# Kernel optimization log

Measured on AMD Instinct MI355X. Metric: run time of the kernel, lower is better.

The kernel has to match this reference:

```python
import jax, jax.numpy as jnp
import numpy as np

B, T, D, H = 16, 256, 128, 256  # batch, max_len, input_size, hidden_size (= attention hidden)


def _gru(x_seq, h0, Wih, Whh, bih, bhh):
    """Torch-style GRU over time. x_seq: [B,T,H_in], h0: [B,H]. Returns outputs [B,T,H], hT [B,H]."""
    x_proj = jnp.einsum('bti,gi->btg', x_seq, Wih) + bih  # [B,T,3H], precompute input projections

    def step(h, xp):
        gi_r, gi_z, gi_n = jnp.split(xp, 3, axis=-1)
        gh = h @ Whh.T + bhh
        gh_r, gh_z, gh_n = jnp.split(gh, 3, axis=-1)
        r = jax.nn.sigmoid(gi_r + gh_r)
        z = jax.nn.sigmoid(gi_z + gh_z)
        n = jnp.tanh(gi_n + r * gh_n)
        h_new = (1.0 - z) * n + z * h
        return h_new, h_new

    hT, outs = jax.lax.scan(step, h0, jnp.swapaxes(x_proj, 0, 1))  # scan over time
    return jnp.swapaxes(outs, 0, 1), hT


def setup_inputs() -> dict:
    key = jax.random.key(0)
    ks = jax.random.split(key, 16)
    s = lambda fan: 1.0 / np.sqrt(fan)
    inp = {
        'inputs': jax.random.normal(ks[0], (B, T, D), dtype=jnp.float32),
        'targets': jax.vmap(lambda k: jax.random.permutation(k, T))(jax.random.split(ks[1], B)).astype(jnp.int64),
        'W_enc': jax.random.normal(ks[2], (H, D), dtype=jnp.float32) * s(D),
        'b_enc': jnp.zeros((H,), dtype=jnp.float32),
        'enc_Wih': jax.random.normal(ks[3], (3 * H, H), dtype=jnp.float32) * s(H),
        'enc_Whh': jax.random.normal(ks[4], (3 * H, H), dtype=jnp.float32) * s(H),
        'enc_bih': jnp.zeros((3 * H,), dtype=jnp.float32),
        'enc_bhh': jnp.zeros((3 * H,), dtype=jnp.float32),
        'dec_Wih': jax.random.normal(ks[5], (3 * H, H), dtype=jnp.float32) * s(H),
        'dec_Whh': jax.random.normal(ks[6], (3 * H, H), dtype=jnp.float32) * s(H),
        'dec_bih': jnp.zeros((3 * H,), dtype=jnp.float32),
        'dec_bhh': jnp.zeros((3 * H,), dtype=jnp.float32),
        'Wq': jax.random.normal(ks[7], (H, H), dtype=jnp.float32) * s(H),
        'Wk': jax.random.normal(ks[8], (H, H), dtype=jnp.float32) * s(H),
        'v': jax.random.normal(ks[9], (H,), dtype=jnp.float32) * s(H),
    }
    return inp


def reference(inputs, targets, W_enc, b_enc, enc_Wih, enc_Whh, enc_bih, enc_bhh,
              dec_Wih, dec_Whh, dec_bih, dec_bhh, Wq, Wk, v):
    # encoder_linear (dropout = 0 at inference)
    enc_in = jnp.einsum('btd,hd->bth', inputs, W_enc) + b_enc  # [B,T,H]
    enc_out, hT = _gru(enc_in, jnp.zeros((B, H), dtype=inputs.dtype), enc_Wih, enc_Whh, enc_bih, enc_bhh)
    # teacher forcing: decoder inputs are encoder_inputs gathered at rolled targets
    dec_idx = jnp.roll(targets, 1, axis=1)  # [B,T]
    dec_rnn_in = jnp.take_along_axis(enc_in, dec_idx[:, :, None], axis=1)  # [B,T,H]
    dec_out, _ = _gru(dec_rnn_in, hT, dec_Wih, dec_Whh, dec_bih, dec_bhh)  # [B,T,H]
    # steps mask: position j available at step t iff j not in targets[:, :t]
    onehot = jax.nn.one_hot(targets, T, dtype=jnp.int32)         # [B,T,T]
    prev = jnp.cumsum(onehot, axis=1) - onehot                   # exclusive cumsum
    steps_mask = prev == 0                                       # [B,T(query),T(key)] bool
    # Bahdanau additive attention: v . tanh(Wq q + Wk k)
    q = jnp.einsum('bth,ah->bta', dec_out, Wq)  # [B,T,A]
    k = jnp.einsum('bsh,ah->bsa', enc_out, Wk)  # [B,S,A]
    scores = jnp.einsum('btsa,a->bts', jnp.tanh(q[:, :, None, :] + k[:, None, :, :]), v)  # [B,T,S]
    logits = jnp.where(steps_mask, scores, jnp.float32(-1e9))
    return logits
```

## Files before the change

kernel.cpp:

```cpp
#include <hip/hip_runtime.h>
#include <hip/hip_fp16.h>

#define B_ 16
#define T_ 256
#define D_ 128
#define H_ 256

typedef _Float16 f16;
typedef __attribute__((ext_vector_type(2))) _Float16 f16x2;
typedef __attribute__((ext_vector_type(4))) int i32x4;

__device__ __forceinline__ float fast_rcp(float x) {
#if __has_builtin(__builtin_amdgcn_rcpf)
    return __builtin_amdgcn_rcpf(x);
#else
    return 1.0f / x;
#endif
}
__device__ __forceinline__ float sigmoid_f(float x) {
    return fast_rcp(1.0f + __expf(-x));
}
__device__ __forceinline__ float tanh_f(float x) {
    float e = __expf(2.0f * x);
    return 1.0f - 2.0f * fast_rcp(1.0f + e);
}
__device__ __forceinline__ float tanh_pade(float x) {
#if __has_builtin(__builtin_amdgcn_fmed3f)
    x = __builtin_amdgcn_fmed3f(x, -4.f, 4.f);
#else
    x = fminf(4.f, fmaxf(-4.f, x));
#endif
    float x2 = x * x;
    return x * (27.f + x2) * fast_rcp(27.f + 9.f * x2);
}
__device__ __forceinline__ int dot8(int a, int b, int c) {
#if __has_builtin(__builtin_amdgcn_sdot8)
    return __builtin_amdgcn_sdot8(a, b, c, false);
#else
    int d;
    asm("v_dot8_i32_i4 %0, %1, %2, %3" : "=v"(d) : "v"(a), "v"(b), "v"(c));
    return d;
#endif
}
template <int CTRL>
__device__ __forceinline__ int dpp_quad(int x) {
    return __builtin_amdgcn_update_dpp(0, x, CTRL, 0xF, 0xF, true);
}
#define DPP_XOR1 0xB1
#define DPP_XOR2 0x4E

__device__ __forceinline__ void gru_phase(const int* __restrict__ w4,
                                          const float* __restrict__ scp,
                                          const float* __restrict__ bhp,
                                          const f16x2* __restrict__ gA,
                                          const f16* __restrict__ gB,
                                          float* __restrict__ outp,
                                          float& hj, int* sh_h4, int tid) {
    const int j = tid >> 1;
    const int hf = tid & 1;
    const float sc0 = scp[j], sc1 = scp[256 + j], sc2 = scp[512 + j];
    const float bn = bhp[512 + j];

    i32x4 wq[3][4];
    {
        unsigned long long base = (unsigned long long)(w4 + tid * 48);
#pragma unroll
        for (int g = 0; g < 3; ++g)
#pragma unroll
            for (int q4 = 0; q4 < 4; ++q4)
                asm volatile("global_load_dwordx4 %0, %1, off offset:%2"
                             : "=v"(wq[g][q4]) : "v"(base), "i"(g * 64 + q4 * 16));
        asm volatile("s_waitcnt vmcnt(0)" ::: "memory");
    }

    f16x2 gab = gA[j];
    f16 gn = gB[j];

    for (int t = 0; t < T_; ++t) {
        const int cur = t & 1;
        int a0 = 0, a1 = 0, a2 = 0;
        const i32x4* hb = (const i32x4*)((const char*)sh_h4 + cur * 128 + hf * 64);
#pragma unroll
        for (int q4 = 0; q4 < 4; ++q4) {
            i32x4 h4 = hb[q4];
#pragma unroll
            for (int d = 0; d < 4; ++d) {
                a0 = dot8(wq[0][q4][d], h4[d], a0);
                a1 = dot8(wq[1][q4][d], h4[d], a1);
                a2 = dot8(wq[2][q4][d], h4[d], a2);
            }
        }
        const int tn = (t < T_ - 1) ? t + 1 : t;
        f16x2 ngab = gA[tn * 256 + j];
        f16 ngn = gB[tn * 256 + j];

        a0 += dpp_quad<DPP_XOR1>(a0);
        a1 += dpp_quad<DPP_XOR1>(a1);
        a2 += dpp_quad<DPP_XOR1>(a2);
        float p0 = (float)a0 * sc0;
        float p1 = (float)a1 * sc1;
        float p2 = (float)a2 * sc2;

        float rr = sigmoid_f((float)gab[0] + p0);
        float zz = sigmoid_f((float)gab[1] + p1);
        float nv = tanh_f((float)gn + rr * (p2 + bn));
        float hn = (1.f - zz) * nv + zz * hj;
        hj = hn;

        if (hf) outp[t * H_ + j] = hn;
        int nib = (int)rintf(hn * 7.f) & 15;
        int hi = dpp_quad<DPP_XOR2>(nib);
        if ((tid & 3) == 0)
            ((char*)sh_h4)[(cur ^ 1) * 128 + (tid >> 2)] = (char)(nib | (hi << 4));

        gab = ngab; gn = ngn;
        asm volatile("s_waitcnt lgkmcnt(0)" ::: "memory");
        __builtin_amdgcn_s_barrier();
    }
}

__global__ __launch_bounds__(256)
void k_prep_pe(const float* __restrict__ wa, const float* __restrict__ wb,
               int* __restrict__ w4a, int* __restrict__ w4b,
               float* __restrict__ sca, float* __restrict__ scb,
               const int* __restrict__ tgt, int* __restrict__ pos,
               const float* __restrict__ inputs,
               const float* __restrict__ Wenc, const float* __restrict__ benc,
               const float* __restrict__ We, const float* __restrict__ bihe,
               const float* __restrict__ bhhe,
               f16x2* __restrict__ giAe, f16* __restrict__ giBe) {
    int blk = blockIdx.x;
    int a = threadIdx.x;
    if (blk < 384) {
        int wid = blk * 4 + (a >> 6);
        int l = a & 63;
        const float* W = wid < 768 ? wa : wb;
        int* w4 = wid < 768 ? w4a : w4b;
        float* sc = wid < 768 ? sca : scb;
        int r = wid & 767;
        int g = r >> 8, j = r & 255;
        const float* Wr = W + r * 256;
        float v[8];
        float m = 0.f;
        if (l < 32) {
#pragma unroll
            for (int q = 0; q < 8; ++q) {
                v[q] = Wr[8 * l + q];
                m = fmaxf(m, fabsf(v[q]));
            }
        }
#pragma unroll
        for (int d = 1; d < 64; d <<= 1) m = fmaxf(m, __shfl_xor(m, d));
        float qs = m > 0.f ? 7.f / m : 0.f;
        if (l == 0) sc[r] = m / 49.f;
        if (l < 32) {
            int pk = 0;
#pragma unroll
            for (int q = 0; q < 8; ++q) pk |= ((int)rintf(v[q] * qs) & 15) << (4 * q);
            int hf = l >> 4, i = l & 15;
            w4[(j * 2 + hf) * 48 + g * 16 + i] = pk;
        }
        return;
    }
    if (blk < 400) {
        __shared__ int pl[256];
        int b = blk - 384;
        pl[a] = T_;
        __syncthreads();
        atomicMin(&pl[tgt[b * 256 + a] & 255], a);
        __syncthreads();
        pos[b * 256 + a] = pl[a];
        return;
    }
    __shared__ float s_in[16][128];
    __shared__ float s_enc[16][256];
    int pblk = blk - 400;
    int bt0 = pblk * 16;
    int b = bt0 >> 8;
    {
        int idx = a * 4 >> 7, k = (a * 4) & 127;
        *(float4*)&s_in[idx][k] = *(const float4*)(inputs + (b * 256 + (bt0 & 255) + idx) * 128 + k);
    }
    {
        int idx = a + 256;
        int row = idx >> 5, k4 = idx & 31;
        ((float4*)s_in[row])[k4] =
            *(const float4*)(inputs + (b * 256 + (bt0 & 255) + row) * 128 + k4 * 4);
    }
    __syncthreads();
#pragma unroll
    for (int it = 0; it < 2; ++it) {
        int idx = a + it * 256;
        int row = idx >> 5, k4 = idx & 31;
        ((float4*)s_in[row])[k4] =
            *(const float4*)(inputs + (b * 256 + (bt0 & 255) + row) * 128 + k4 * 4);
    }
    __syncthreads();
    {
        float eacc[16];
#pragma unroll
        for (int tt = 0; tt < 16; ++tt) eacc[tt] = benc[a];
        const float* wr = Wenc + a * 128;
        for (int k = 0; k < 128; k += 4) {
            float4 w4 = *(const float4*)(wr + k);
#pragma unroll
            for (int tt = 0; tt < 16; ++tt) {
                float4 x4 = *(const float4*)&s_in[tt][k];
                eacc[tt] += w4.x * x4.x + w4.y * x4.y + w4.z * x4.z + w4.w * x4.w;
            }
        }
#pragma unroll
        for (int tt = 0; tt < 16; ++tt) s_enc[tt][a] = eacc[tt];
    }
    __syncthreads();
    float acc0[16], acc1[16], acc2[16];
    float b0 = bihe[a] + bhhe[a];
    float b1 = bihe[a + 256] + bhhe[a + 256];
    float b2 = bihe[a + 512];
#pragma unroll
    for (int tt = 0; tt < 16; ++tt) { acc0[tt] = b0; acc1[tt] = b1; acc2[tt] = b2; }
    const float* w0 = We + a * H_;
    const float* w1 = We + (a + 256) * H_;
    const float* w2 = We + (a + 512) * H_;
    for (int k = 0; k < H_; k += 4) {
        float4 a4 = *(const float4*)(w0 + k);
        float4 b4 = *(const float4*)(w1 + k);
        float4 c4 = *(const float4*)(w2 + k);
#pragma unroll
        for (int tt = 0; tt < 16; ++tt) {
            float4 x4 = *(const float4*)&s_enc[tt][k];
            acc0[tt] += a4.x * x4.x + a4.y * x4.y + a4.z * x4.z + a4.w * x4.w;
            acc1[tt] += b4.x * x4.x + b4.y * x4.y + b4.z * x4.z + b4.w * x4.w;
            acc2[tt] += c4.x * x4.x + c4.y * x4.y + c4.z * x4.z + c4.w * x4.w;
        }
    }
#pragma unroll
    for (int tt = 0; tt < 16; ++tt) {
        int row = bt0 + tt;
        giAe[row * 256 + a] = (f16x2){(f16)acc0[tt], (f16)acc1[tt]};
        giBe[row * 256 + a] = (f16)acc2[tt];
    }
}

__global__ __launch_bounds__(512)
__attribute__((amdgpu_waves_per_eu(2, 2)))
void k_egru_pd(const int* __restrict__ w4e, const float* __restrict__ sce,
               const f16x2* __restrict__ giAe, const f16* __restrict__ giBe,
               const float* __restrict__ bhhe,
               float* __restrict__ enc_out, float* __restrict__ hT,
               const float* __restrict__ inputs,
               const float* __restrict__ Wenc, const float* __restrict__ benc,
               const float* __restrict__ Wd, const float* __restrict__ bihd,
               const float* __restrict__ bhhd, const int* __restrict__ tgt,
               f16x2* __restrict__ giAd, f16* __restrict__ giBd) {
    __shared__ __align__(16) int sh_h4[2][32];
    __shared__ float s_in[32][128];
    __shared__ float s_enc[32][256];
    const int blk = blockIdx.x;
    const int tid = threadIdx.x;
    if (blk < 16) {
        const int m = blk;
        if (tid < 64) ((int*)sh_h4)[tid] = 0;
        float hj = 0.f;
        __syncthreads();
        gru_phase(w4e, sce, bhhe, giAe + m * (T_ * 256), giBe + m * (T_ * 256),
                  enc_out + m * (T_ * H_), hj, &sh_h4[0][0], tid);
        if (tid & 1) hT[m * H_ + (tid >> 1)] = hj;
        return;
    }
    const int pblk = blk - 16;
    const int bt0 = pblk * 32;
    const int b = bt0 >> 8;
    const int a = tid & 255;
    const int half = tid >> 8;
    int tsrc[16];
#pragma unroll
    for (int i = 0; i < 16; ++i) {
        int t = (bt0 & 255) + half * 16 + i;
        tsrc[i] = tgt[(b << 8) + ((t + 255) & 255)] & 255;
    }
#pragma unroll
    for (int it = 0; it < 2; ++it) {
        int idx = tid + it * 512;
        int row = idx >> 5, k4 = idx & 31;
        int t = (bt0 & 255) + row;
        int rs = tgt[(b << 8) + ((t + 255) & 255)] & 255;
        ((float4*)s_in[row])[k4] = *(const float4*)(inputs + (b * 256 + rs) * 128 + k4 * 4);
    }
    __syncthreads();
    {
        float eacc[16];
#pragma unroll
        for (int i = 0; i < 16; ++i) eacc[i] = benc[a];
        const float* wr = Wenc + a * 128;
        for (int k = 0; k < 128; k += 4) {
            float4 w4 = *(const float4*)(wr + k);
#pragma unroll
            for (int i = 0; i < 16; ++i) {
                float4 x4 = *(const float4*)&s_in[half * 16 + i][k];
                eacc[i] += w4.x * x4.x + w4.y * x4.y + w4.z * x4.z + w4.w * x4.w;
            }
        }
#pragma unroll
        for (int i = 0; i < 16; ++i) s_enc[half * 16 + i][a] = eacc[i];
    }
    __syncthreads();
    float acc0[16], acc1[16], acc2[16];
    float b0 = bihd[a] + bhhd[a];
    float b1 = bihd[a + 256] + bhhd[a + 256];
    float b2 = bihd[a + 512];
#pragma unroll
    for (int i = 0; i < 16; ++i) { acc0[i] = b0; acc1[i] = b1; acc2[i] = b2; }
    const float* w0 = Wd + a * H_;
    const float* w1 = Wd + (a + 256) * H_;
    const float* w2 = Wd + (a + 512) * H_;
    for (int k = 0; k < H_; k += 4) {
        float4 a4 = *(const float4*)(w0 + k);
        float4 b4 = *(const float4*)(w1 + k);
        float4 c4 = *(const float4*)(w2 + k);
#pragma unroll
        for (int i = 0; i < 16; ++i) {
            float4 x4 = *(const float4*)&s_enc[half * 16 + i][k];
            acc0[i] += a4.x * x4.x + a4.y * x4.y + a4.z * x4.z + a4.w * x4.w;
            acc1[i] += b4.x * x4.x + b4.y * x4.y + b4.z * x4.z + b4.w * x4.w;
            acc2[i] += c4.x * x4.x + c4.y * x4.y + c4.z * x4.z + c4.w * x4.w;
        }
    }
#pragma unroll
    for (int i = 0; i < 16; ++i) {
        int row = bt0 + half * 16 + i;
        giAd[row * 256 + a] = (f16x2){(f16)acc0[i], (f16)acc1[i]};
        giBd[row * 256 + a] = (f16)acc2[i];
    }
    (void)tsrc;
}

__global__ __launch_bounds__(512)
__attribute__((amdgpu_waves_per_eu(2, 2)))
void k_dgru_kt(const int* __restrict__ w4d, const float* __restrict__ scd,
               const f16x2* __restrict__ giAd, const f16* __restrict__ giBd,
               const float* __restrict__ bhhd,
               float* __restrict__ dec_out, const float* __restrict__ hT,
               const float* __restrict__ enc_out, const float* __restrict__ Wk,
               float* __restrict__ kT) {
    __shared__ __align__(16) int sh_h4[2][32];
    __shared__ float tile[32][256];
    const int blk = blockIdx.x;
    const int tid = threadIdx.x;
    if (blk < 16) {
        const int m = blk;
        const int j = tid >> 1;
        float hj = hT[m * H_ + j];
        int nib = (int)rintf(hj * 7.f) & 15;
        int hi = dpp_quad<DPP_XOR2>(nib);
        if ((tid & 3) == 0)
            ((char*)sh_h4)[tid >> 2] = (char)(nib | (hi << 4));
        __syncthreads();
        gru_phase(w4d, scd, bhhd, giAd + m * (T_ * 256), giBd + m * (T_ * 256),
                  dec_out + m * (T_ * H_), hj, &sh_h4[0][0], tid);
        return;
    }
    const int kblk = blk - 16;
    const int bt0 = kblk * 32;
    const int b = bt0 >> 8, s0 = bt0 & 255;
    const int a = tid & 255;
    const int half = tid >> 8;
    float acc[16];
#pragma unroll
    for (int i = 0; i < 16; ++i) acc[i] = 0.f;
    const float* w0 = Wk + a * H_;
    for (int k = 0; k < H_; k += 4) {
        float4 w4 = *(const float4*)(w0 + k);
#pragma unroll
        for (int i = 0; i < 16; ++i) {
            float4 x4 = *(const float4*)(enc_out + (bt0 + half * 16 + i) * H_ + k);
            acc[i] += w4.x * x4.x + w4.y * x4.y + w4.z * x4.z + w4.w * x4.w;
        }
    }
#pragma unroll
    for (int i = 0; i < 16; ++i) tile[half * 16 + i][a] = acc[i];
    __syncthreads();
#pragma unroll
    for (int i4 = 0; i4 < 4; ++i4) {
        float4 f = {tile[half * 16 + i4 * 4 + 0][a], tile[half * 16 + i4 * 4 + 1][a],
                    tile[half * 16 + i4 * 4 + 2][a], tile[half * 16 + i4 * 4 + 3][a]};
        *(float4*)(kT + b * (T_ * H_) + a * T_ + s0 + half * 16 + i4 * 4) = f;
    }
}

__global__ __launch_bounds__(256) void k_q(const float* __restrict__ dec_out,
                                           const float* __restrict__ Wq,
                                           float* __restrict__ q) {
    int bt0 = blockIdx.x * 16;
    int a = threadIdx.x;
    float acc[16];
#pragma unroll
    for (int tt = 0; tt < 16; ++tt) acc[tt] = 0.f;
    const float* w0 = Wq + a * H_;
    for (int k = 0; k < H_; k += 4) {
        float4 w4 = *(const float4*)(w0 + k);
#pragma unroll
        for (int tt = 0; tt < 16; ++tt) {
            float4 x4 = *(const float4*)(dec_out + (bt0 + tt) * H_ + k);
            acc[tt] += w4.x * x4.x + w4.y * x4.y + w4.z * x4.z + w4.w * x4.w;
        }
    }
#pragma unroll
    for (int tt = 0; tt < 16; ++tt) q[(bt0 + tt) * H_ + a] = acc[tt];
}

__global__ __launch_bounds__(256) void k_scores(const float* __restrict__ q,
                                                const float* __restrict__ kT,
                                                const float* __restrict__ v,
                                                const int* __restrict__ pos,
                                                float* __restrict__ out) {
    __shared__ float sq[4][256];
    __shared__ float sv[256];
    int blk = blockIdx.x;
    int b = blk >> 6;
    int t0 = (blk & 63) * 4;
    int s = threadIdx.x;
    sv[s] = v[s];
#pragma unroll
    for (int tt = 0; tt < 4; ++tt)
        sq[tt][s] = q[((b << 8) + t0 + tt) * H_ + s];
    __syncthreads();
    int ps = pos[(b << 8) + s];
    float acc[4] = {0.f, 0.f, 0.f, 0.f};
    const float* kTb = kT + b * (T_ * H_);
    for (int a = 0; a < H_; ++a) {
        float kv = kTb[a * T_ + s];
        float va = sv[a];
#pragma unroll
        for (int tt = 0; tt < 4; ++tt) {
            float th = tanh_pade(sq[tt][a] + kv);
            acc[tt] += va * th;
        }
    }
#pragma unroll
    for (int tt = 0; tt < 4; ++tt) {
        int t = t0 + tt;
        out[((b << 8) + t) * T_ + s] = (t <= ps) ? acc[tt] : -1.0e9f;
    }
}

extern "C" void kernel_launch(void* const* d_in, const int* in_sizes, int n_in,
                              void* d_out, int out_size, void* d_ws, size_t ws_size,
                              hipStream_t stream) {
    (void)in_sizes; (void)n_in; (void)out_size; (void)ws_size;
    const float* inputs   = (const float*)d_in[0];
    const int* targets    = (const int*)d_in[1];
    const float* W_enc   = (const float*)d_in[2];
    const float* b_enc   = (const float*)d_in[3];
    const float* enc_Wih = (const float*)d_in[4];
    const float* enc_Whh = (const float*)d_in[5];
    const float* enc_bih = (const float*)d_in[6];
    const float* enc_bhh = (const float*)d_in[7];
    const float* dec_Wih = (const float*)d_in[8];
    const float* dec_Whh = (const float*)d_in[9];
    const float* dec_bih = (const float*)d_in[10];
    const float* dec_bhh = (const float*)d_in[11];
    const float* Wq = (const float*)d_in[12];
    const float* Wk = (const float*)d_in[13];
    const float* v  = (const float*)d_in[14];
    float* out = (float*)d_out;

    float* ws = (float*)d_ws;
    f16x2* giAe    = (f16x2*)ws;
    f16*   giBe    = (f16*)(ws + 1048576);
    f16x2* giAd    = (f16x2*)(ws + 1572864);
    f16*   giBd    = (f16*)(ws + 2621440);
    float* enc_out = ws + 3145728;
    float* dec_out = ws + 4194304;
    int*   w4e     = (int*)(ws + 5242880);
    int*   w4d     = (int*)(ws + 5292032);
    float* sce     = ws + 5341184;
    float* scd     = ws + 5341952;
    int*   pos     = (int*)(ws + 5342720);
    float* hT      = ws + 5346816;
    float* kT = (float*)giAe;
    float* q  = (float*)giAd;

    k_prep_pe<<<656, 256, 0, stream>>>(enc_Whh, dec_Whh, w4e, w4d, sce, scd,
                                       targets, pos, inputs, W_enc, b_enc,
                                       enc_Wih, enc_bih, enc_bhh, giAe, giBe);
    k_egru_pd<<<144, 512, 0, stream>>>(w4e, sce, giAe, giBe, enc_bhh, enc_out, hT,
                                       inputs, W_enc, b_enc,
                                       dec_Wih, dec_bih, dec_bhh, targets,
                                       giAd, giBd);
    k_dgru_kt<<<144, 512, 0, stream>>>(w4d, scd, giAd, giBd, dec_bhh, dec_out, hT,
                                       enc_out, Wk, kT);
    k_q<<<256, 256, 0, stream>>>(dec_out, Wq, q);
    k_scores<<<1024, 256, 0, stream>>>(q, kT, v, pos, out);
}
```

Before: 412.7 us.

## Fuse query projection into attention scores kernel and drop redundant loads

New measurement: 460.1 us. 11.5% more time.

```diff
diff --git a/kernel.cpp b/kernel.cpp
--- a/kernel.cpp
+++ b/kernel.cpp
@@ -177,17 +177,6 @@
     int pblk = blk - 400;
     int bt0 = pblk * 16;
     int b = bt0 >> 8;
-    {
-        int idx = a * 4 >> 7, k = (a * 4) & 127;
-        *(float4*)&s_in[idx][k] = *(const float4*)(inputs + (b * 256 + (bt0 & 255) + idx) * 128 + k);
-    }
-    {
-        int idx = a + 256;
-        int row = idx >> 5, k4 = idx & 31;
-        ((float4*)s_in[row])[k4] =
-            *(const float4*)(inputs + (b * 256 + (bt0 & 255) + row) * 128 + k4 * 4);
-    }
-    __syncthreads();
 #pragma unroll
     for (int it = 0; it < 2; ++it) {
         int idx = a + it * 256;
@@ -273,12 +262,6 @@
     const int b = bt0 >> 8;
     const int a = tid & 255;
     const int half = tid >> 8;
-    int tsrc[16];
-#pragma unroll
-    for (int i = 0; i < 16; ++i) {
-        int t = (bt0 & 255) + half * 16 + i;
-        tsrc[i] = tgt[(b << 8) + ((t + 255) & 255)] & 255;
-    }
 #pragma unroll
     for (int it = 0; it < 2; ++it) {
         int idx = tid + it * 512;
@@ -332,7 +315,6 @@
         giAd[row * 256 + a] = (f16x2){(f16)acc0[i], (f16)acc1[i]};
         giBd[row * 256 + a] = (f16)acc2[i];
     }
-    (void)tsrc;
 }
 
 __global__ __launch_bounds__(512)
@@ -388,57 +370,60 @@
     }
 }
 
-__global__ __launch_bounds__(256) void k_q(const float* __restrict__ dec_out,
-                                           const float* __restrict__ Wq,
-                                           float* __restrict__ q) {
-    int bt0 = blockIdx.x * 16;
-    int a = threadIdx.x;
-    float acc[16];
-#pragma unroll
-    for (int tt = 0; tt < 16; ++tt) acc[tt] = 0.f;
-    const float* w0 = Wq + a * H_;
-    for (int k = 0; k < H_; k += 4) {
-        float4 w4 = *(const float4*)(w0 + k);
-#pragma unroll
-        for (int tt = 0; tt < 16; ++tt) {
-            float4 x4 = *(const float4*)(dec_out + (bt0 + tt) * H_ + k);
-            acc[tt] += w4.x * x4.x + w4.y * x4.y + w4.z * x4.z + w4.w * x4.w;
-        }
-    }
-#pragma unroll
-    for (int tt = 0; tt < 16; ++tt) q[(bt0 + tt) * H_ + a] = acc[tt];
-}
-
-__global__ __launch_bounds__(256) void k_scores(const float* __restrict__ q,
-                                                const float* __restrict__ kT,
-                                                const float* __restrict__ v,
-                                                const int* __restrict__ pos,
-                                                float* __restrict__ out) {
-    __shared__ float sq[4][256];
+__global__ __launch_bounds__(256) void k_qscores(const float* __restrict__ dec_out,
+                                                 const float* __restrict__ Wq,
+                                                 const float* __restrict__ kT,
+                                                 const float* __restrict__ v,
+                                                 const int* __restrict__ pos,
+                                                 float* __restrict__ out) {
+    __shared__ float sdec[16][256];
+    __shared__ float sq[16][256];
     __shared__ float sv[256];
     int blk = blockIdx.x;
-    int b = blk >> 6;
-    int t0 = (blk & 63) * 4;
+    int b = blk >> 4;
+    int t0 = (blk & 15) * 16;
     int s = threadIdx.x;
     sv[s] = v[s];
-#pragma unroll
-    for (int tt = 0; tt < 4; ++tt)
-        sq[tt][s] = q[((b << 8) + t0 + tt) * H_ + s];
+    {
+#pragma uno
+#pragma unroll
+        for (int tt = 0; tt < 16; ++tt)
+            sdec[tt][s] = dec_out[((b << 8) + t0 + tt) * H_ + s];
+    }
+    __syncthreads();
+    {
+        float qa[16];
+#pragma unroll
+        for (int tt = 0; tt < 16; ++tt) qa[tt] = 0.f;
+        const float* wq = Wq + s * H_;
+        for (int k = 0; k < H_; k += 4) {
+            float4 w4 = *(const float4*)(wq + k);
+#pragma unroll
+            for (int tt = 0; tt < 16; ++tt) {
+                float4 x4 = *(const float4*)&sdec[tt][k];
+                qa[tt] += w4.x * x4.x + w4.y * x4.y + w4.z * x4.z + w4.w * x4.w;
+            }
+        }
+#pragma unroll
+        for (int tt = 0; tt < 16; ++tt) sq[tt][s] = qa[tt];
+    }
     __syncthreads();
     int ps = pos[(b << 8) + s];
-    float acc[4] = {0.f, 0.f, 0.f, 0.f};
+    float acc[16];
+#pragma unroll
+    for (int tt = 0; tt < 16; ++tt) acc[tt] = 0.f;
     const float* kTb = kT + b * (T_ * H_);
     for (int a = 0; a < H_; ++a) {
         float kv = kTb[a * T_ + s];
         float va = sv[a];
 #pragma unroll
-        for (int tt = 0; tt < 4; ++tt) {
+        for (int tt = 0; tt < 16; ++tt) {
             float th = tanh_pade(sq[tt][a] + kv);
             acc[tt] += va * th;
         }
     }
 #pragma unroll
-    for (int tt = 0; tt < 4; ++tt) {
+    for (int tt = 0; tt < 16; ++tt) {
         int t = t0 + tt;
         out[((b << 8) + t) * T_ + s] = (t <= ps) ? acc[tt] : -1.0e9f;
     }
@@ -479,7 +464,6 @@
     int*   pos     = (int*)(ws + 5342720);
     float* hT      = ws + 5346816;
     float* kT = (float*)giAe;
-    float* q  = (float*)giAd;
 
     k_prep_pe<<<656, 256, 0, stream>>>(enc_Whh, dec_Whh, w4e, w4d, sce, scd,
                                        targets, pos, inputs, W_enc, b_enc,
@@ -490,6 +474,5 @@
                                        giAd, giBd);
     k_dgru_kt<<<144, 512, 0, stream>>>(w4d, scd, giAd, giBd, dec_bhh, dec_out, hT,
                                        enc_out, Wk, kT);
-    k_q<<<256, 256, 0, stream>>>(dec_out, Wq, q);
-    k_scores<<<1024, 256, 0, stream>>>(q, kT, v, pos, out);
-}
+    k_qscores<<<256, 256, 0, stream>>>(dec_out, Wq, kT, v, pos, out);
+}
```
